# Kernel optimization log

Measured on AMD Instinct MI355X. Metric: run time of the kernel, lower is better.

The kernel has to match this reference:

```python
import jax, jax.numpy as jnp
import numpy as np

B, N, C, H = 16, 1029, 1024, 16
D = C // H  # head_dim = 64
N_ROPE = 1024  # patch tokens covered by rope; prefix = N - N_ROPE = 5


def setup_inputs() -> dict:
    key = jax.random.key(0)
    ks = jax.random.split(key, 8)
    x = jax.random.normal(ks[0], (B, N, C), dtype=jnp.float32)
    rope_sin = jax.random.uniform(ks[1], (N_ROPE, D), dtype=jnp.float32, minval=-1.0, maxval=1.0)
    rope_cos = jax.random.uniform(ks[2], (N_ROPE, D), dtype=jnp.float32, minval=-1.0, maxval=1.0)
    s = 1.0 / np.sqrt(C)
    W_qkv = jax.random.normal(ks[3], (3 * C, C), dtype=jnp.float32) * s
    b_qkv = jax.random.normal(ks[4], (3 * C,), dtype=jnp.float32) * 0.02
    W_proj = jax.random.normal(ks[5], (C, C), dtype=jnp.float32) * s
    b_proj = jax.random.normal(ks[6], (C,), dtype=jnp.float32) * 0.02
    return {"x": x, "rope_sin": rope_sin, "rope_cos": rope_cos,
            "W_qkv": W_qkv, "b_qkv": b_qkv, "W_proj": W_proj, "b_proj": b_proj}


def _rotate_half(t):
    t1, t2 = jnp.split(t, 2, axis=-1)
    return jnp.concatenate([-t2, t1], axis=-1)


def _rope_apply(t, sin, cos):
    # t: [B, H, N_rope, D]; sin/cos: [N_rope, D] broadcast over B, H
    return t * cos + _rotate_half(t) * sin


def reference(x, rope_sin, rope_cos, W_qkv, b_qkv, W_proj, b_proj):
    b, n, c = x.shape
    h, d = H, c // H
    # QKV projection (torch Linear: x @ W.T + b)
    qkv = x @ W_qkv.T + b_qkv                       # [B, N, 3C]
    qkv = qkv.reshape(b, n, 3, h, d)
    q = jnp.transpose(qkv[:, :, 0], (0, 2, 1, 3))   # [B, H, N, D]
    k = jnp.transpose(qkv[:, :, 1], (0, 2, 1, 3))
    v = jnp.transpose(qkv[:, :, 2], (0, 2, 1, 3))
    # RoPE on the patch-token suffix only
    prefix = n - rope_sin.shape[-2]
    q = jnp.concatenate([q[:, :, :prefix], _rope_apply(q[:, :, prefix:], rope_sin, rope_cos)], axis=2)
    k = jnp.concatenate([k[:, :, :prefix], _rope_apply(k[:, :, prefix:], rope_sin, rope_cos)], axis=2)
    # Scaled dot-product attention (default scale = 1/sqrt(D))
    scale = 1.0 / jnp.sqrt(jnp.asarray(d, dtype=x.dtype))
    scores = jnp.einsum('bhqd,bhkd->bhqk', q, k) * scale
    attn = jax.nn.softmax(scores, axis=-1)
    out = jnp.einsum('bhqk,bhkd->bhqd', attn, v)    # [B, H, N, D]
    out = jnp.transpose(out, (0, 2, 1, 3)).reshape(b, n, c)
    # Output projection
    return out @ W_proj.T + b_proj
```

## Files before the change

### kernel.cpp

```cpp
#include <hip/hip_runtime.h>
#include <cfloat>
#include <math.h>

#define B_      16
#define N_TOK   1029
#define C_      1024
#define H_      16
#define D_      64
#define PREFIX  5
#define M_ROWS  (B_ * N_TOK)
#define HEAD_SLAB ((size_t)B_ * H_ * N_TOK * D_)
#define VT_STRIDE 1088

typedef __attribute__((ext_vector_type(8))) short bf16x8;
typedef __attribute__((ext_vector_type(4))) float f32x4;

__device__ __forceinline__ unsigned short f2bf(float f) {
    unsigned u = __float_as_uint(f);
    u += 0x7fffu + ((u >> 16) & 1u);
    return (unsigned short)(u >> 16);
}
__device__ __forceinline__ float bf2f(unsigned short h) {
    return __uint_as_float(((unsigned)h) << 16);
}

__global__ __launch_bounds__(256)
void split_kernel(const float* __restrict__ in, unsigned short* __restrict__ hi,
                  unsigned short* __restrict__ lo, int n4)
{
    const int i = blockIdx.x * 256 + threadIdx.x;
    if (i >= n4) return;
    const float4 v = ((const float4*)in)[i];
    ushort4 h, l;
    h.x = f2bf(v.x); l.x = f2bf(v.x - bf2f(h.x));
    h.y = f2bf(v.y); l.y = f2bf(v.y - bf2f(h.y));
    h.z = f2bf(v.z); l.z = f2bf(v.z - bf2f(h.z));
    h.w = f2bf(v.w); l.w = f2bf(v.w - bf2f(h.w));
    ((ushort4*)hi)[i] = h;
    ((ushort4*)lo)[i] = l;
}

__device__ __forceinline__ bf16x8 frag_ld(const unsigned short* slab, int r, int q) {
    const int L = r >> 1;
    const int s = (q | ((r & 1) << 2)) ^ (L & 7);
    return *(const bf16x8*)(slab + L * 64 + s * 8);
}

#define WAIT_BAR(N) do {                                          \
    asm volatile("s_waitcnt vmcnt(" #N ")" ::: "memory");         \
    __builtin_amdgcn_s_barrier();                                 \
    __builtin_amdgcn_sched_barrier(0);                            \
} while (0)

__global__ __launch_bounds__(512, 2)
void gemm_mfma8(const unsigned short* __restrict__ Ahi, const unsigned short* __restrict__ Alo,
                const unsigned short* __restrict__ Whi, const unsigned short* __restrict__ Wlo,
                const float* __restrict__ bias, float* __restrict__ out,
                int M, int Ncols, int K, int scatter)
{
    __shared__ unsigned short lds[2][4][256 * 32];

    const int tid  = threadIdx.x;
    const int wave = tid >> 6;
    const int lane = tid & 63;
    const int lm   = lane & 15;
    const int quad = lane >> 4;
    const int bx = blockIdx.x, by = blockIdx.y;
    const int wm = wave >> 2;
    const int wn = wave & 3;
    const int rowA = by * 256;
    const int rowB = bx * 256;

    f32x4 acc[8][4];
#pragma unroll
    for (int mi = 0; mi < 8; ++mi)
#pragma unroll
        for (int ni = 0; ni < 4; ++ni)
            acc[mi][ni] = (f32x4){0.f, 0.f, 0.f, 0.f};

#define STAGE(buf_, slab_, base_, row0_, doClamp_, k0_) do {                          \
    _Pragma("unroll")                                                                 \
    for (int i_ = 0; i_ < 2; ++i_) {                                                  \
        const int c_ = i_ * 512 + tid;                                                \
        const int L_ = c_ >> 3;                                                       \
        const int u_ = (c_ & 7) ^ (L_ & 7);                                           \
        int grow_ = (row0_) + 2 * L_ + (u_ >> 2);                                     \
        if (doClamp_) grow_ = min(grow_, M - 1);                                      \
        const unsigned short* src_ = (base_) + (size_t)grow_ * K + (k0_) + (u_ & 3) * 8; \
        __builtin_amdgcn_global_load_lds(                                             \
            (__attribute__((address_space(1))) void*)src_,                            \
            (__attribute__((address_space(3))) void*)&lds[buf_][slab_][(i_ * 512 + wave * 64) * 8], \
            16, 0, 0);                                                                \
    }                                                                                 \
} while (0)

    STAGE(0, 0, Ahi, rowA, true,  0);
    STAGE(0, 2, Whi, rowB, false, 0);
    STAGE(0, 3, Wlo, rowB, false, 0);
    STAGE(0, 1, Alo, rowA, true,  0);

    const int NT = K >> 5;
    for (int t = 0; t < NT; ++t) {
        const int cur = t & 1, nxt = cur ^ 1;
        const int tn = (t + 1 == NT) ? 0 : t + 1;
        const int k1 = tn << 5;

        WAIT_BAR(4);
        STAGE(nxt, 0, Ahi, rowA, true,  k1);
        STAGE(nxt, 2, Whi, rowB, false, k1);
        bf16x8 b[4], a[8];
#pragma unroll
        for (int ni = 0; ni < 4; ++ni)
            b[ni] = frag_ld(&lds[cur][2][0], wn * 64 + ni * 16 + lm, quad);
#pragma unroll
        for (int mi = 0; mi < 8; ++mi)
            a[mi] = frag_ld(&lds[cur][0][0], wm * 128 + mi * 16 + lm, quad);
        __builtin_amdgcn_s_setprio(1);
#pragma unroll
        for (int mi = 0; mi < 8; ++mi)
#pragma unroll
            for (int ni = 0; ni < 4; ++ni)
                acc[mi][ni] = __builtin_amdgcn_mfma_f32_16x16x32_bf16(a[mi], b[ni], acc[mi][ni], 0, 0, 0);
        __builtin_amdgcn_s_setprio(0);

        WAIT_BAR(6);
        STAGE(nxt, 3, Wlo, rowB, false, k1);
        __builtin_amdgcn_s_setprio(1);
#pragma unroll
        for (int ni = 0; ni < 4; ++ni) {
            const bf16x8 bl = frag_ld(&lds[cur][3][0], wn * 64 + ni * 16 + lm, quad);
#pragma unroll
            for (int mi = 0; mi < 8; ++mi)
                acc[mi][ni] = __builtin_amdgcn_mfma_f32_16x16x32_bf16(a[mi], bl, acc[mi][ni], 0, 0, 0);
        }
        __builtin_amdgcn_s_setprio(0);

        WAIT_BAR(6);
        STAGE(nxt, 1, Alo, rowA, true, k1);
        __builtin_amdgcn_s_setprio(1);
#pragma unroll
        for (int mi = 0; mi < 8; ++mi) {
            const bf16x8 al = frag_ld(&lds[cur][1][0], wm * 128 + mi * 16 + lm, quad);
#pragma unroll
            for (int ni = 0; ni < 4; ++ni)
                acc[mi][ni] = __builtin_amdgcn_mfma_f32_16x16x32_bf16(al, b[ni], acc[mi][ni], 0, 0, 0);
        }
        __builtin_amdgcn_s_setprio(0);
    }
#undef STAGE
    asm volatile("s_waitcnt vmcnt(0)" ::: "memory");

#pragma unroll
    for (int mi = 0; mi < 8; ++mi) {
#pragma unroll
        for (int rr = 0; rr < 4; ++rr) {
            const int gm = rowA + wm * 128 + mi * 16 + quad * 4 + rr;
            if (gm >= M) continue;
            if (!scatter) {
#pragma unroll
                for (int ni = 0; ni < 4; ++ni) {
                    const int gn = rowB + wn * 64 + ni * 16 + lm;
                    out[(size_t)gm * Ncols + gn] = acc[mi][ni][rr] + bias[gn];
                }
            } else {
                const int b_  = gm / N_TOK;
                const int tok = gm - b_ * N_TOK;
#pragma unroll
                for (int ni = 0; ni < 4; ++ni) {
                    const int gn    = rowB + wn * 64 + ni * 16 + lm;
                    const int which = gn >> 10;
                    const int h     = (gn >> 6) & 15;
                    const int d     = gn & 63;
                    const size_t dst = (size_t)which * HEAD_SLAB +
                                       (((size_t)(b_ * H_ + h)) * N_TOK + tok) * 64 + d;
                    out[dst] = acc[mi][ni][rr] + bias[gn];
                }
            }
        }
    }
}
#undef WAIT_BAR

__global__ __launch_bounds__(256)
void rope_convert(const float* __restrict__ qf, const float* __restrict__ kf,
                  const float* __restrict__ sin_, const float* __restrict__ cos_,
                  unsigned short* __restrict__ qhi, unsigned short* __restrict__ qlo,
                  unsigned short* __restrict__ khi, unsigned short* __restrict__ klo)
{
    const int idx = blockIdx.x * 256 + threadIdx.x;
    const int total = B_ * H_ * N_TOK * 32;
    if (idx >= total) return;
    const int d   = idx & 31;
    const int tmp = idx >> 5;
    const int n   = tmp % N_TOK;
    const int bh  = tmp / N_TOK;

    const size_t base = ((size_t)bh * N_TOK + n) * 64;
    float q1 = qf[base + d], q2 = qf[base + d + 32];
    float k1 = kf[base + d], k2 = kf[base + d + 32];

    if (n >= PREFIX) {
        const int r = n - PREFIX;
        const float c1 = cos_[r * 64 + d];
        const float c2 = cos_[r * 64 + d + 32];
        const float s1 = sin_[r * 64 + d];
        const float s2 = sin_[r * 64 + d + 32];
        const float nq1 = q1 * c1 - q2 * s1;
        const float nq2 = q2 * c2 + q1 * s2;
        q1 = nq1; q2 = nq2;
        const float nk1 = k1 * c1 - k2 * s1;
        const float nk2 = k2 * c2 + k1 * s2;
        k1 = nk1; k2 = nk2;
    }
    q1 *= 0.125f; q2 *= 0.125f;

    unsigned short h;
    h = f2bf(q1); qhi[base + d]      = h; qlo[base + d]      = f2bf(q1 - bf2f(h));
    h = f2bf(q2); qhi[base + d + 32] = h; qlo[base + d + 32] = f2bf(q2 - bf2f(h));
    h = f2bf(k1); khi[base + d]      = h; klo[base + d]      = f2bf(k1 - bf2f(h));
    h = f2bf(k2); khi[base + d + 32] = h; klo[base + d + 32] = f2bf(k2 - bf2f(h));
}

__global__ __launch_bounds__(256)
void v_transpose(const float* __restrict__ vf, unsigned short* __restrict__ vt)
{
    __shared__ float t[64][65];
    const int tid = threadIdx.x;
    const int kt0 = blockIdx.x * 64;
    const int bh  = blockIdx.y;
    const float* src = vf + (size_t)bh * N_TOK * 64;

#pragma unroll
    for (int p = 0; p < 4; ++p) {
        const int e   = p * 256 + tid;
        const int key = e >> 4;
        const int c4  = (e & 15) << 2;
        const int gk  = kt0 + key;
        float4 v = make_float4(0.f, 0.f, 0.f, 0.f);
        if (gk < N_TOK) v = *(const float4*)(src + (size_t)gk * 64 + c4);
        t[key][c4 + 0] = v.x;
        t[key][c4 + 1] = v.y;
        t[key][c4 + 2] = v.z;
        t[key][c4 + 3] = v.w;
    }
    __syncthreads();

    const int d  = tid >> 2;
    const int kb = (tid & 3) << 4;
    unsigned short buf[16];
#pragma unroll
    for (int j = 0; j < 16; ++j) buf[j] = f2bf(t[kb + j][d]);
    unsigned short* dst = vt + (size_t)bh * 64 * VT_STRIDE + (size_t)d * VT_STRIDE + kt0 + kb;
#pragma unroll
    for (int j = 0; j < 4; ++j)
        *(ushort4*)(dst + j * 4) = *(ushort4*)&buf[j * 4];
}

__global__ __launch_bounds__(256, 2)
void attn_mfma2(const unsigned short* __restrict__ qhi_g, const unsigned short* __restrict__ qlo_g,
                const unsigned short* __restrict__ khi_g, const unsigned short* __restrict__ klo_g,
                const unsigned short* __restrict__ vt_g,
                unsigned short* __restrict__ Ohi, unsigned short* __restrict__ Olo)
{
    __shared__ unsigned short Khl[2][64 * 64];
    __shared__ unsigned short Kll[2][64 * 64];
    __shared__ unsigned short Vtl[2][64 * 64];
    __shared__ unsigned short Pl[128 * 64];

    const int tid  = threadIdx.x;
    const int wave = tid >> 6;
    const int lane = tid & 63;
    const int lm   = lane & 15;
    const int quad = lane >> 4;
    const int bh   = blockIdx.x;
    const int q0   = blockIdx.y * 128;
    const int b    = bh >> 4;
    const int h    = bh & 15;

    const unsigned short* Qh  = qhi_g + (size_t)bh * N_TOK * 64;
    const unsigned short* Ql  = qlo_g + (size_t)bh * N_TOK * 64;
    const unsigned short* Khb = khi_g + (size_t)bh * N_TOK * 64;
    const unsigned short* Klb = klo_g + (size_t)bh * N_TOK * 64;
    const unsigned short* Vtb = vt_g  + (size_t)bh * 64 * VT_STRIDE;

#define STAGE(bs, kt0_) do {                                                     \
    _Pragma("unroll")                                                            \
    for (int pass = 0; pass < 2; ++pass) {                                       \
        const int t  = pass * 256 + tid;                                         \
        const int r  = t >> 3;                                                   \
        const int qs = t & 7;                                                    \
        const int sw = (qs ^ (r & 7)) << 3;                                      \
        const int ldsoff = (pass * 256 + wave * 64) * 8;                         \
        const int gk = min((kt0_) + r, N_TOK - 1);                               \
        __builtin_amdgcn_global_load_lds(                                        \
            (__attribute__((address_space(1))) void*)(Khb + (size_t)gk * 64 + sw), \
            (__attribute__((address_space(3))) void*)&Khl[bs][ldsoff], 16, 0, 0);  \
        __builtin_amdgcn_global_load_lds(                                        \
            (__attribute__((address_space(1))) void*)(Klb + (size_t)gk * 64 + sw), \
            (__attribute__((address_space(3))) void*)&Kll[bs][ldsoff], 16, 0, 0);  \
        __builtin_amdgcn_global_load_lds(                                        \
            (__attribute__((address_space(1))) void*)(Vtb + (size_t)r * VT_STRIDE + (kt0_) + sw), \
            (__attribute__((address_space(3))) void*)&Vtl[bs][ldsoff], 16, 0, 0);  \
    }                                                                            \
} while (0)

    STAGE(0, 0);

    bf16x8 qh[2][2], ql[2][2];
#pragma unroll
    for (int rt = 0; rt < 2; ++rt) {
        int row = q0 + wave * 32 + rt * 16 + lm;
        if (row > N_TOK - 1) row = N_TOK - 1;
#pragma unroll
        for (int s = 0; s < 2; ++s) {
            const size_t off = (size_t)row * 64 + s * 32 + quad * 8;
            qh[rt][s] = *(const bf16x8*)&Qh[off];
            ql[rt][s] = *(const bf16x8*)&Ql[off];
        }
    }

    f32x4 o[2][4];
    float m_i[2][4], l_i[2][4];
#pragma unroll
    for (int rt = 0; rt < 2; ++rt)
#pragma unroll
        for (int r = 0; r < 4; ++r) {
            m_i[rt][r] = -FLT_MAX;
            l_i[rt][r] = 0.f;
            o[rt][r] = (f32x4){0.f, 0.f, 0.f, 0.f};
        }

    asm volatile("s_waitcnt vmcnt(0)\n\ts_barrier" ::: "memory");

    for (int kt = 0; kt < 17; ++kt) {
        const int kt0 = kt * 64;
        const int cur = kt & 1;

        if (kt < 16) STAGE(cur ^ 1, kt0 + 64);

        f32x4 s_acc[2][4];
#pragma unroll
        for (int rt = 0; rt < 2; ++rt)
#pragma unroll
            for (int ct = 0; ct < 4; ++ct)
                s_acc[rt][ct] = (f32x4){0.f, 0.f, 0.f, 0.f};

#pragma unroll
        for (int ct = 0; ct < 4; ++ct) {
            const int krow = ct * 16 + lm;
#pragma unroll
            for (int s = 0; s < 2; ++s) {
                const int chunk = ((s * 4 + quad) ^ (krow & 7)) << 3;
                const bf16x8 kbh = *(const bf16x8*)&Khl[cur][krow * 64 + chunk];
                const bf16x8 kbl = *(const bf16x8*)&Kll[cur][krow * 64 + chunk];
#pragma unroll
                for (int rt = 0; rt < 2; ++rt) {
                    s_acc[rt][ct] = __builtin_amdgcn_mfma_f32_16x16x32_bf16(qh[rt][s], kbh, s_acc[rt][ct], 0, 0, 0);
                    s_acc[rt][ct] = __builtin_amdgcn_mfma_f32_16x16x32_bf16(qh[rt][s], kbl, s_acc[rt][ct], 0, 0, 0);
                    s_acc[rt][ct] = __builtin_amdgcn_mfma_f32_16x16x32_bf16(ql[rt][s], kbh, s_acc[rt][ct], 0, 0, 0);
                }
            }
        }

        if (kt0 + 64 > N_TOK) {
#pragma unroll
            for (int ct = 0; ct < 4; ++ct) {
                if (kt0 + ct * 16 + lm >= N_TOK) {
#pragma unroll
                    for (int rt = 0; rt < 2; ++rt)
#pragma unroll
                        for (int r = 0; r < 4; ++r) s_acc[rt][ct][r] = -FLT_MAX;
                }
            }
        }

#pragma unroll
        for (int rt = 0; rt < 2; ++rt) {
#pragma unroll
            for (int r = 0; r < 4; ++r) {
                float mt = fmaxf(fmaxf(s_acc[rt][0][r], s_acc[rt][1][r]),
                                 fmaxf(s_acc[rt][2][r], s_acc[rt][3][r]));
                mt = fmaxf(mt, __shfl_xor(mt, 1));
                mt = fmaxf(mt, __shfl_xor(mt, 2));
                mt = fmaxf(mt, __shfl_xor(mt, 4));
                mt = fmaxf(mt, __shfl_xor(mt, 8));
                const float mnew  = fmaxf(m_i[rt][r], mt);
                const float alpha = __expf(m_i[rt][r] - mnew);
                float pv[4], rs = 0.f;
#pragma unroll
                for (int ct = 0; ct < 4; ++ct) {
                    pv[ct] = __expf(s_acc[rt][ct][r] - mnew);
                    rs += pv[ct];
                }
                rs += __shfl_xor(rs, 1);
                rs += __shfl_xor(rs, 2);
                rs += __shfl_xor(rs, 4);
                rs += __shfl_xor(rs, 8);
                l_i[rt][r] = l_i[rt][r] * alpha + rs;
                m_i[rt][r] = mnew;
#pragma unroll
                for (int dt = 0; dt < 4; ++dt) o[rt][dt][r] *= alpha;
                const int prow = wave * 32 + rt * 16 + quad * 4 + r;
#pragma unroll
                for (int ct = 0; ct < 4; ++ct) {
                    const int col = ct * 16 + lm;
                    const int idx = prow * 64 + ((((col >> 3) ^ (prow & 7)) << 3) | (col & 7));
                    Pl[idx] = f2bf(pv[ct]);
                }
            }
        }

#pragma unroll
        for (int ks = 0; ks < 2; ++ks) {
            bf16x8 pf[2];
#pragma unroll
            for (int rt = 0; rt < 2; ++rt) {
                const int prow = wave * 32 + rt * 16 + lm;
                const int chunk = ((ks * 4 + quad) ^ (prow & 7)) << 3;
                pf[rt] = *(const bf16x8*)&Pl[prow * 64 + chunk];
            }
#pragma unroll
            for (int dt = 0; dt < 4; ++dt) {
                const int vrow = dt * 16 + lm;
                const int chunk = ((ks * 4 + quad) ^ (vrow & 7)) << 3;
                const bf16x8 vh = *(const bf16x8*)&Vtl[cur][vrow * 64 + chunk];
#pragma unroll
                for (int rt = 0; rt < 2; ++rt)
                    o[rt][dt] = __builtin_amdgcn_mfma_f32_16x16x32_bf16(pf[rt], vh, o[rt][dt], 0, 0, 0);
            }
        }

        asm volatile("s_waitcnt vmcnt(0)\n\ts_barrier" ::: "memory");
    }
#undef STAGE

#pragma unroll
    for (int rt = 0; rt < 2; ++rt) {
#pragma unroll
        for (int r = 0; r < 4; ++r) {
            const int gq = q0 + wave * 32 + rt * 16 + quad * 4 + r;
            if (gq >= N_TOK) continue;
            const float inv = 1.0f / l_i[rt][r];
            const size_t base = (((size_t)(b * N_TOK + gq)) * H_ + h) * D_;
#pragma unroll
            for (int dt = 0; dt < 4; ++dt) {
                const float val = o[rt][dt][r] * inv;
                const unsigned short hb = f2bf(val);
                Ohi[base + dt * 16 + lm] = hb;
                Olo[base + dt * 16 + lm] = f2bf(val - bf2f(hb));
            }
        }
    }
}

extern "C" void kernel_launch(void* const* d_in, const int* in_sizes, int n_in,
                              void* d_out, int out_size, void* d_ws, size_t ws_size,
                              hipStream_t stream)
{
    const float* x        = (const float*)d_in[0];
    const float* rope_sin = (const float*)d_in[1];
    const float* rope_cos = (const float*)d_in[2];
    const float* W_qkv    = (const float*)d_in[3];
    const float* b_qkv    = (const float*)d_in[4];
    const float* W_proj   = (const float*)d_in[5];
    const float* b_proj   = (const float*)d_in[6];
    float* out = (float*)d_out;

    float* q_buf = (float*)d_ws;
    float* k_buf = q_buf + HEAD_SLAB;
    float* v_buf = q_buf + 2 * HEAD_SLAB;
    float* slab4 = q_buf + 3 * HEAD_SLAB;

    unsigned short* x_hi = (unsigned short*)slab4;
    unsigned short* x_lo = x_hi + HEAD_SLAB;
    unsigned short* wq_hi = (unsigned short*)d_out;
    unsigned short* wq_lo = wq_hi + (size_t)3 * C_ * C_;

    unsigned short* vthi  = (unsigned short*)d_out;
    unsigned short* qhi   = (unsigned short*)v_buf;
    unsigned short* qlo   = qhi + HEAD_SLAB;
    unsigned short* khi   = (unsigned short*)slab4;
    unsigned short* klo   = khi + HEAD_SLAB;
    unsigned short* attn_hi = (unsigned short*)q_buf;
    unsigned short* attn_lo = attn_hi + HEAD_SLAB;
    unsigned short* wp_hi = (unsigned short*)k_buf;
    unsigned short* wp_lo = wp_hi + (size_t)C_ * C_;

    {
        const int n4x = M_ROWS * C_ / 4;
        split_kernel<<<(n4x + 255) / 256, 256, 0, stream>>>(x, x_hi, x_lo, n4x);
        const int n4q = 3 * C_ * C_ / 4;
        split_kernel<<<(n4q + 255) / 256, 256, 0, stream>>>(W_qkv, wq_hi, wq_lo, n4q);
    }
    {
        dim3 grid(3 * C_ / 256, (M_ROWS + 255) / 256);
        gemm_mfma8<<<grid, 512, 0, stream>>>(x_hi, x_lo, wq_hi, wq_lo, b_qkv,
                                             q_buf, M_ROWS, 3 * C_, C_, 1);
    }
    {
        dim3 grid(17, B_ * H_);
        v_transpose<<<grid, 256, 0, stream>>>(v_buf, vthi);
    }
    {
        const int total = B_ * H_ * N_TOK * 32;
        rope_convert<<<(total + 255) / 256, 256, 0, stream>>>(
            q_buf, k_buf, rope_sin, rope_cos, qhi, qlo, khi, klo);
    }
    {
        dim3 grid(B_ * H_, (N_TOK + 127) / 128);
        attn_mfma2<<<grid, 256, 0, stream>>>(qhi, qlo, khi, klo, vthi,
                                             attn_hi, attn_lo);
    }
    {
        const int n4p = C_ * C_ / 4;
        split_kernel<<<(n4p + 255) / 256, 256, 0, stream>>>(W_proj, wp_hi, wp_lo, n4p);
    }
    {
        dim3 grid(C_ / 256, (M_ROWS + 255) / 256);
        gemm_mfma8<<<grid, 512, 0, stream>>>(attn_hi, attn_lo, wp_hi, wp_lo, b_proj,
                                             out, M_ROWS, C_, C_, 0);
    }
}
```

Baseline: 944.8 us.

## Use 8 waves of 16 query rows each in attention kernel instead of 4x32

The attention block now launches 512 threads, with each wave owning 16 query rows rather than 32. K/V tile staging drops to a single pass per thread, and per-wave register state for Q, O and the scores is halved. The aim is more waves per CU to hide latency, at the cost of each K/V LDS fragment load feeding only half as many MFMAs, so there is less register-level reuse.

```diff
diff --git a/kernel.cpp b/kernel.cpp
--- a/kernel.cpp
+++ b/kernel.cpp
@@ -256,7 +256,7 @@
         *(ushort4*)(dst + j * 4) = *(ushort4*)&buf[j * 4];
 }
 
-__global__ __launch_bounds__(256, 2)
+__global__ __launch_bounds__(512, 4)
 void attn_mfma2(const unsigned short* __restrict__ qhi_g, const unsigned short* __restrict__ qlo_g,
                 const unsigned short* __restrict__ khi_g, const unsigned short* __restrict__ klo_g,
                 const unsigned short* __restrict__ vt_g,
@@ -284,51 +284,44 @@
     const unsigned short* Vtb = vt_g  + (size_t)bh * 64 * VT_STRIDE;
 
 #define STAGE(bs, kt0_) do {                                                     \
-    _Pragma("unroll")                                                            \
-    for (int pass = 0; pass < 2; ++pass) {                                       \
-        const int t  = pass * 256 + tid;                                         \
-        const int r  = t >> 3;                                                   \
-        const int qs = t & 7;                                                    \
-        const int sw = (qs ^ (r & 7)) << 3;                                      \
-        const int ldsoff = (pass * 256 + wave * 64) * 8;                         \
-        const int gk = min((kt0_) + r, N_TOK - 1);                               \
-        __builtin_amdgcn_global_load_lds(                                        \
-            (__attribute__((address_space(1))) void*)(Khb + (size_t)gk * 64 + sw), \
-            (__attribute__((address_space(3))) void*)&Khl[bs][ldsoff], 16, 0, 0);  \
-        __builtin_amdgcn_global_load_lds(                                        \
-            (__attribute__((address_space(1))) void*)(Klb + (size_t)gk * 64 + sw), \
-            (__attribute__((address_space(3))) void*)&Kll[bs][ldsoff], 16, 0, 0);  \
-        __builtin_amdgcn_global_load_lds(                                        \
-            (__attribute__((address_space(1))) void*)(Vtb + (size_t)r * VT_STRIDE + (kt0_) + sw), \
-            (__attribute__((address_space(3))) void*)&Vtl[bs][ldsoff], 16, 0, 0);  \
-    }                                                                            \
+    const int r_  = tid >> 3;                                                    \
+    const int qs_ = tid & 7;                                                     \
+    const int sw_ = (qs_ ^ (r_ & 7)) << 3;                                       \
+    const int ldsoff_ = wave * 512;                                              \
+    const int gk_ = min((kt0_) + r_, N_TOK - 1);                                 \
+    __builtin_amdgcn_global_load_lds(                                            \
+        (__attribute__((address_space(1))) void*)(Khb + (size_t)gk_ * 64 + sw_), \
+        (__attribute__((address_space(3))) void*)&Khl[bs][ldsoff_], 16, 0, 0);   \
+    __builtin_amdgcn_global_load_lds(                                            \
+        (__attribute__((address_space(1))) void*)(Klb + (size_t)gk_ * 64 + sw_), \
+        (__attribute__((address_space(3))) void*)&Kll[bs][ldsoff_], 16, 0, 0);   \
+    __builtin_amdgcn_global_load_lds(                                            \
+        (__attribute__((address_space(1))) void*)(Vtb + (size_t)r_ * VT_STRIDE + (kt0_) + sw_), \
+        (__attribute__((address_space(3))) void*)&Vtl[bs][ldsoff_], 16, 0, 0);   \
 } while (0)
 
     STAGE(0, 0);
 
-    bf16x8 qh[2][2], ql[2][2];
-#pragma unroll
-    for (int rt = 0; rt < 2; ++rt) {
-        int row = q0 + wave * 32 + rt * 16 + lm;
+    bf16x8 qh[2], ql[2];
+    {
+        int row = q0 + wave * 16 + lm;
         if (row > N_TOK - 1) row = N_TOK - 1;
 #pragma unroll
         for (int s = 0; s < 2; ++s) {
             const size_t off = (size_t)row * 64 + s * 32 + quad * 8;
-            qh[rt][s] = *(const bf16x8*)&Qh[off];
-            ql[rt][s] = *(const bf16x8*)&Ql[off];
-        }
-    }
-
-    f32x4 o[2][4];
-    float m_i[2][4], l_i[2][4];
-#pragma unroll
-    for (int rt = 0; rt < 2; ++rt)
-#pragma unroll
-        for (int r = 0; r < 4; ++r) {
-            m_i[rt][r] = -FLT_MAX;
-            l_i[rt][r] = 0.f;
-            o[rt][r] = (f32x4){0.f, 0.f, 0.f, 0.f};
-        }
+            qh[s] = *(const bf16x8*)&Qh[off];
+            ql[s] = *(const bf16x8*)&Ql[off];
+        }
+    }
+
+    f32x4 o[4];
+    float m_i[4], l_i[4];
+#pragma unroll
+    for (int r = 0; r < 4; ++r) {
+        m_i[r] = -FLT_MAX;
+        l_i[r] = 0.f;
+        o[r] = (f32x4){0.f, 0.f, 0.f, 0.f};
+    }
 
     asm volatile("s_waitcnt vmcnt(0)\n\ts_barrier" ::: "memory");
 
@@ -338,12 +331,10 @@
 
         if (kt < 16) STAGE(cur ^ 1, kt0 + 64);
 
-        f32x4 s_acc[2][4];
-#pragma unroll
-        for (int rt = 0; rt < 2; ++rt)
-#pragma unroll
-            for (int ct = 0; ct < 4; ++ct)
-                s_acc[rt][ct] = (f32x4){0.f, 0.f, 0.f, 0.f};
+        f32x4 s_acc[4];
+#pragma unroll
+        for (int ct = 0; ct < 4; ++ct)
+            s_acc[ct] = (f32x4){0.f, 0.f, 0.f, 0.f};
 
 #pragma unroll
         for (int ct = 0; ct < 4; ++ct) {
@@ -353,12 +344,9 @@
                 const int chunk = ((s * 4 + quad) ^ (krow & 7)) << 3;
                 const bf16x8 kbh = *(const bf16x8*)&Khl[cur][krow * 64 + chunk];
                 const bf16x8 kbl = *(const bf16x8*)&Kll[cur][krow * 64 + chunk];
-#pragma unroll
-                for (int rt = 0; rt < 2; ++rt) {
-                    s_acc[rt][ct] = __builtin_amdgcn_mfma_f32_16x16x32_bf16(qh[rt][s], kbh, s_acc[rt][ct], 0, 0, 0);
-                    s_acc[rt][ct] = __builtin_amdgcn_mfma_f32_16x16x32_bf16(qh[rt][s], kbl, s_acc[rt][ct], 0, 0, 0);
-                    s_acc[rt][ct] = __builtin_amdgcn_mfma_f32_16x16x32_bf16(ql[rt][s], kbh, s_acc[rt][ct], 0, 0, 0);
-                }
+                s_acc[ct] = __builtin_amdgcn_mfma_f32_16x16x32_bf16(qh[s], kbh, s_acc[ct], 0, 0, 0);
+                s_acc[ct] = __builtin_amdgcn_mfma_f32_16x16x32_bf16(qh[s], kbl, s_acc[ct], 0, 0, 0);
+                s_acc[ct] = __builtin_amdgcn_mfma_f32_16x16x32_bf16(ql[s], kbh, s_acc[ct], 0, 0, 0);
             }
         }
 
@@ -367,66 +355,55 @@
             for (int ct = 0; ct < 4; ++ct) {
                 if (kt0 + ct * 16 + lm >= N_TOK) {
 #pragma unroll
-                    for (int rt = 0; rt < 2; ++rt)
-#pragma unroll
-                        for (int r = 0; r < 4; ++r) s_acc[rt][ct][r] = -FLT_MAX;
+                    for (int r = 0; r < 4; ++r) s_acc[ct][r] = -FLT_MAX;
                 }
             }
         }
 
 #pragma unroll
-        for (int rt = 0; rt < 2; ++rt) {
-#pragma unroll
-            for (int r = 0; r < 4; ++r) {
-                float mt = fmaxf(fmaxf(s_acc[rt][0][r], s_acc[rt][1][r]),
-                                 fmaxf(s_acc[rt][2][r], s_acc[rt][3][r]));
-                mt = fmaxf(mt, __shfl_xor(mt, 1));
-                mt = fmaxf(mt, __shfl_xor(mt, 2));
-                mt = fmaxf(mt, __shfl_xor(mt, 4));
-                mt = fmaxf(mt, __shfl_xor(mt, 8));
-                const float mnew  = fmaxf(m_i[rt][r], mt);
-                const float alpha = __expf(m_i[rt][r] - mnew);
-                float pv[4], rs = 0.f;
-#pragma unroll
-                for (int ct = 0; ct < 4; ++ct) {
-                    pv[ct] = __expf(s_acc[rt][ct][r] - mnew);
-                    rs += pv[ct];
-                }
-                rs += __shfl_xor(rs, 1);
-                rs += __shfl_xor(rs, 2);
-                rs += __shfl_xor(rs, 4);
-                rs += __shfl_xor(rs, 8);
-                l_i[rt][r] = l_i[rt][r] * alpha + rs;
-                m_i[rt][r] = mnew;
-#pragma unroll
-                for (int dt = 0; dt < 4; ++dt) o[rt][dt][r] *= alpha;
-                const int prow = wave * 32 + rt * 16 + quad * 4 + r;
-#pragma unroll
-                for (int ct = 0; ct < 4; ++ct) {
-                    const int col = ct * 16 + lm;
-                    const int idx = prow * 64 + ((((col >> 3) ^ (prow & 7)) << 3) | (col & 7));
-                    Pl[idx] = f2bf(pv[ct]);
-                }
+        for (int r = 0; r < 4; ++r) {
+            float mt = fmaxf(fmaxf(s_acc[0][r], s_acc[1][r]),
+                             fmaxf(s_acc[2][r], s_acc[3][r]));
+            mt = fmaxf(mt, __shfl_xor(mt, 1));
+            mt = fmaxf(mt, __shfl_xor(mt, 2));
+            mt = fmaxf(mt, __shfl_xor(mt, 4));
+            mt = fmaxf(mt, __shfl_xor(mt, 8));
+            const float mnew  = fmaxf(m_i[r], mt);
+            const float alpha = __expf(m_i[r] - mnew);
+            float pv[4], rs = 0.f;
+#pragma unroll
+            for (int ct = 0; ct < 4; ++ct) {
+                pv[ct] = __expf(s_acc[ct][r] - mnew);
+                rs += pv[ct];
+            }
+            rs += __shfl_xor(rs, 1);
+            rs += __shfl_xor(rs, 2);
+            rs += __shfl_xor(rs, 4);
+            rs += __shfl_xor(rs, 8);
+            l_i[r] = l_i[r] * alpha + rs;
+            m_i[r] = mnew;
+#pragma unroll
+            for (int dt = 0; dt < 4; ++dt) o[dt][r] *= alpha;
+            const int prow = wave * 16 + quad * 4 + r;
+#pragma unroll
+            for (int ct = 0; ct < 4; ++ct) {
+                const int col = ct * 16 + lm;
+                const int idx = prow * 64 + ((((col >> 3) ^ (prow & 7)) << 3) | (col & 7));
+                Pl[idx] = f2bf(pv[ct]);
             }
         }
 
 #pragma unroll
         for (int ks = 0; ks < 2; ++ks) {
-            bf16x8 pf[2];
-#pragma unroll
-            for (int rt = 0; rt < 2; ++rt) {
-                const int prow = wave * 32 + rt * 16 + lm;
-                const int chunk = ((ks * 4 + quad) ^ (prow & 7)) << 3;
-                pf[rt] = *(const bf16x8*)&Pl[prow * 64 + chunk];
-            }
+            const int prow = wave * 16 + lm;
+            const int chunk = ((ks * 4 + quad) ^ (prow & 7)) << 3;
+            const bf16x8 pf = *(const bf16x8*)&Pl[prow * 64 + chunk];
 #pragma unroll
             for (int dt = 0; dt < 4; ++dt) {
                 const int vrow = dt * 16 + lm;
-                const int chunk = ((ks * 4 + quad) ^ (vrow & 7)) << 3;
-                const bf16x8 vh = *(const bf16x8*)&Vtl[cur][vrow * 64 + chunk];
-#pragma unroll
-                for (int rt = 0; rt < 2; ++rt)
-                    o[rt][dt] = __builtin_amdgcn_mfma_f32_16x16x32_bf16(pf[rt], vh, o[rt][dt], 0, 0, 0);
+                const int chunkv = ((ks * 4 + quad) ^ (vrow & 7)) << 3;
+                const bf16x8 vh = *(const bf16x8*)&Vtl[cur][vrow * 64 + chunkv];
+                o[dt] = __builtin_amdgcn_mfma_f32_16x16x32_bf16(pf, vh, o[dt], 0, 0, 0);
             }
         }
 
@@ -435,20 +412,17 @@
 #undef STAGE
 
 #pragma unroll
-    for (int rt = 0; rt < 2; ++rt) {
-#pragma unroll
-        for (int r = 0; r < 4; ++r) {
-            const int gq = q0 + wave * 32 + rt * 16 + quad * 4 + r;
-            if (gq >= N_TOK) continue;
-            const float inv = 1.0f / l_i[rt][r];
-            const size_t base = (((size_t)(b * N_TOK + gq)) * H_ + h) * D_;
-#pragma unroll
-            for (int dt = 0; dt < 4; ++dt) {
-                const float val = o[rt][dt][r] * inv;
-                const unsigned short hb = f2bf(val);
-                Ohi[base + dt * 16 + lm] = hb;
-                Olo[base + dt * 16 + lm] = f2bf(val - bf2f(hb));
-            }
+    for (int r = 0; r < 4; ++r) {
+        const int gq = q0 + wave * 16 + quad * 4 + r;
+        if (gq >= N_TOK) continue;
+        const float inv = 1.0f / l_i[r];
+        const size_t base = (((size_t)(b * N_TOK + gq)) * H_ + h) * D_;
+#pragma unroll
+        for (int dt = 0; dt < 4; ++dt) {
+            const float val = o[dt][r] * inv;
+            const unsigned short hb = f2bf(val);
+            Ohi[base + dt * 16 + lm] = hb;
+            Olo[base + dt * 16 + lm] = f2bf(val - bf2f(hb));
         }
     }
 }
@@ -508,7 +482,7 @@
     }
     {
         dim3 grid(B_ * H_, (N_TOK + 127) / 128);
-        attn_mfma2<<<grid, 256, 0, stream>>>(qhi, qlo, khi, klo, vthi,
+        attn_mfma2<<<grid, 512, 0, stream>>>(qhi, qlo, khi, klo, vthi,
                                              attn_hi, attn_lo);
     }
     {
```

After: 947.1 us. Within noise of the previous version (+0.2%).
